# Performance work log

Hardware: AMD Instinct MI355X
Metric: run time of the kernel (lower is better)

Reference implementation:

```python
import jax, jax.numpy as jnp
import numpy as np

B, S, D, H = 1, 2048, 2048, 32
HD = D // H  # head_dim = 64
FF = 4 * D
EPS = 1e-5


def _alibi_slopes(n_heads):
    # standard ALiBi slopes for power-of-2 head counts: 2^(-8i/n)
    return np.array([2.0 ** (-8.0 * (i + 1) / n_heads) for i in range(n_heads)], np.float32)


def setup_inputs() -> dict:
    key = jax.random.key(0)
    ks = jax.random.split(key, 16)
    s = 0.02
    x = jax.random.normal(ks[0], (B, S, D), jnp.float32)
    # alibi bias [B, H, 1, S], broadcast over query positions (HF views alibi as (b, h, 1, kv_len))
    slopes = _alibi_slopes(H)
    alibi_np = slopes[:, None, None] * np.arange(S, dtype=np.float32)[None, None, :]
    alibi = jnp.broadcast_to(jnp.asarray(alibi_np), (B, H, 1, S))
    # additive causal mask [1, 1, S, S]
    causal = np.tril(np.ones((S, S), bool))
    attention_mask = jnp.asarray(np.where(causal, 0.0, -1e9).astype(np.float32))[None, None]
    p = lambda k, shp: s * jax.random.normal(k, shp, jnp.float32)
    return {
        "x": x,
        "alibi": alibi,
        "attention_mask": attention_mask,
        "ln1_g": jnp.ones((D,), jnp.float32), "ln1_b": jnp.zeros((D,), jnp.float32),
        "ln2_g": jnp.ones((D,), jnp.float32), "ln2_b": jnp.zeros((D,), jnp.float32),
        "wqkv": p(ks[1], (D, 3 * D)), "bqkv": jnp.zeros((3 * D,), jnp.float32),
        "wo": p(ks[2], (D, D)), "bo": jnp.zeros((D,), jnp.float32),
        "w1": p(ks[3], (D, FF)), "b1": jnp.zeros((FF,), jnp.float32),
        "w2": p(ks[4], (FF, D)), "b2": jnp.zeros((D,), jnp.float32),
    }


def _layernorm(h, g, b):
    m = h.mean(-1, keepdims=True)
    v = ((h - m) ** 2).mean(-1, keepdims=True)
    return (h - m) * jax.lax.rsqrt(v + EPS) * g + b


def reference(x, alibi, attention_mask, ln1_g, ln1_b, ln2_g, ln2_b,
              wqkv, bqkv, wo, bo, w1, b1, w2, b2):
    b, s, d = x.shape
    inv_norm = 1.0 / np.sqrt(HD).astype(np.float32)
    # --- input layernorm ---
    h = _layernorm(x, ln1_g, ln1_b)
    # --- fused QKV ---
    qkv = h @ wqkv + bqkv
    q, k, v = jnp.split(qkv, 3, axis=-1)
    q = q.reshape(b, s, H, HD).transpose(0, 2, 1, 3)  # [b, h, s, hd]
    k = k.reshape(b, s, H, HD).transpose(0, 2, 1, 3)
    v = v.reshape(b, s, H, HD).transpose(0, 2, 1, 3)
    # --- ALiBi-biased attention (HF falcon alibi path) ---
    scores = jnp.einsum("bhqd,bhkd->bhqk", q, k)          # [b, h, s, s]
    logits = (scores + alibi) * inv_norm + attention_mask  # alibi broadcasts over q dim
    probs = jax.nn.softmax(logits, axis=-1)
    ctx = jnp.einsum("bhqk,bhkd->bhqd", probs, v)
    ctx = ctx.transpose(0, 2, 1, 3).reshape(b, s, d)
    attn_out = ctx @ wo + bo
    # --- residual, post-attn layernorm, MLP (non-parallel falcon-rw layout) ---
    res = x + attn_out
    h2 = _layernorm(res, ln2_g, ln2_b)
    mlp = jax.nn.gelu(h2 @ w1 + b1, approximate=False) @ w2 + b2
    return res + mlp
```

## Files before the change

kernel.cpp:

```cpp
#include <hip/hip_runtime.h>
#include <hip/hip_bf16.h>
#include <cstdint>
#include <cstddef>

static constexpr int Sq  = 2048;
static constexpr int Dm  = 2048;
static constexpr int NH  = 32;
static constexpr int HDm = 64;
static constexpr int FFm = 8192;

typedef __bf16 bf16x8 __attribute__((ext_vector_type(8)));
typedef float  f32x4  __attribute__((ext_vector_type(4)));

__device__ __forceinline__ void async_ld16(const void* g, void* l) {
  __builtin_amdgcn_global_load_lds((const __attribute__((address_space(1))) void*)g,
                                   (__attribute__((address_space(3))) void*)l, 16, 0, 0);
}

__global__ __launch_bounds__(256)
void tcast_kernel(const float* __restrict__ in, __hip_bfloat16* __restrict__ out,
                  int K, int N) {
  __shared__ float tile[64][65];
  const int tc = blockIdx.x * 64;
  const int tr = blockIdx.y * 64;
  const int cx = threadIdx.x & 63;
  const int ry = threadIdx.x >> 6;
#pragma unroll
  for (int i = 0; i < 16; ++i) {
    int r = ry + i * 4;
    tile[r][cx] = in[(size_t)(tr + r) * N + tc + cx];
  }
  __syncthreads();
#pragma unroll
  for (int i = 0; i < 16; ++i) {
    int r = ry + i * 4;
    out[(size_t)(tc + r) * K + tr + cx] = __float2bfloat16(tile[cx][r]);
  }
}

__global__ __launch_bounds__(256)
void ln_kernel(const float* __restrict__ x, const float* __restrict__ g,
               const float* __restrict__ b, __hip_bfloat16* __restrict__ out) {
  __shared__ float red[4];
  const int t = threadIdx.x;
  const float* xr = x + (size_t)blockIdx.x * Dm;
  float v[8];
  float s = 0.f;
#pragma unroll
  for (int i = 0; i < 8; ++i) { v[i] = xr[t + i * 256]; s += v[i]; }
#pragma unroll
  for (int off = 32; off > 0; off >>= 1) s += __shfl_down(s, off, 64);
  if ((t & 63) == 0) red[t >> 6] = s;
  __syncthreads();
  const float mean = (red[0] + red[1] + red[2] + red[3]) * (1.f / Dm);
  __syncthreads();
  float vs = 0.f;
#pragma unroll
  for (int i = 0; i < 8; ++i) { float d = v[i] - mean; vs += d * d; }
#pragma unroll
  for (int off = 32; off > 0; off >>= 1) vs += __shfl_down(vs, off, 64);
  if ((t & 63) == 0) red[t >> 6] = vs;
  __syncthreads();
  const float inv = rsqrtf((red[0] + red[1] + red[2] + red[3]) * (1.f / Dm) + 1e-5f);
  __hip_bfloat16* orow = out + (size_t)blockIdx.x * Dm;
#pragma unroll
  for (int i = 0; i < 8; ++i) {
    int c = t + i * 256;
    orow[c] = __float2bfloat16((v[i] - mean) * inv * g[c] + b[c]);
  }
}

template <int EPI>
__global__ __launch_bounds__(256)
void gemm_kernel(const __hip_bfloat16* __restrict__ A,
                 const __hip_bfloat16* __restrict__ Bt,
                 int N, int K, int Ksub,
                 const float* __restrict__ bias,
                 const float* __restrict__ addsrc,
                 float* __restrict__ outf,
                 __hip_bfloat16* __restrict__ outb,
                 __hip_bfloat16* __restrict__ qo,
                 __hip_bfloat16* __restrict__ ko,
                 __hip_bfloat16* __restrict__ vo,
                 __hip_bfloat16* __restrict__ po) {
  __shared__ __align__(16) __hip_bfloat16 As[2][128 * 32];
  __shared__ __align__(16) __hip_bfloat16 Bs[2][128 * 32];
  const int t = threadIdx.x;
  const int lane = t & 63, w = t >> 6, quad = lane >> 4, l16 = lane & 15;
  const int bn = blockIdx.x, bm = blockIdx.y, bz = blockIdx.z;
  const int wm = (w & 1) * 64, wn = (w >> 1) * 64;
  const __hip_bfloat16* Abase = A + (size_t)bm * 128 * K;
  const __hip_bfloat16* Bbase = Bt + (size_t)bn * 128 * K;
  const int kBeg = bz * Ksub, kEnd = kBeg + Ksub;

  auto stage = [&](int b, int k0) {
#pragma unroll
    for (int j = 0; j < 2; ++j) {
      int c = j * 256 + t;
      int row = c >> 2;
      int p = c & 3;
      int g = (p - (row >> 1)) & 3;
      async_ld16(Abase + (size_t)row * K + k0 + g * 8, &As[b][c * 8]);
      async_ld16(Bbase + (size_t)row * K + k0 + g * 8, &Bs[b][c * 8]);
    }
  };

  f32x4 acc[4][4] = {};
  stage(0, kBeg);
  int buf = 0;
  for (int k0 = kBeg; k0 < kEnd; k0 += 32, buf ^= 1) {
    __syncthreads();
    if (k0 + 32 < kEnd) stage(buf ^ 1, k0 + 32);
    bf16x8 af[4], bfv[4];
#pragma unroll
    for (int i = 0; i < 4; ++i) {
      int row = wm + i * 16 + l16;
      int p = (quad + (row >> 1)) & 3;
      af[i] = *(const bf16x8*)(&As[buf][row * 32 + p * 8]);
    }
#pragma unroll
    for (int i = 0; i < 4; ++i) {
      int row = wn + i * 16 + l16;
      int p = (quad + (row >> 1)) & 3;
      bfv[i] = *(const bf16x8*)(&Bs[buf][row * 32 + p * 8]);
    }
#pragma unroll
    for (int mt = 0; mt < 4; ++mt)
#pragma unroll
      for (int nt = 0; nt < 4; ++nt)
        acc[mt][nt] = __builtin_amdgcn_mfma_f32_16x16x32_bf16(af[mt], bfv[nt], acc[mt][nt], 0, 0, 0);
  }
#pragma unroll
  for (int mt = 0; mt < 4; ++mt) {
#pragma unroll
    for (int nt = 0; nt < 4; ++nt) {
      const int n = bn * 128 + wn + nt * 16 + l16;
      const float bz2 = bias[n];
#pragma unroll
      for (int r = 0; r < 4; ++r) {
        const int m = bm * 128 + wm + mt * 16 + quad * 4 + r;
        float val = acc[mt][nt][r];
        if constexpr (EPI == 0) {
          val += bz2;
          int which = n >> 11, d2 = n & 2047;
          int hh = d2 >> 6, hd = d2 & 63;
          if (which == 0)
            qo[((size_t)hh * Sq + m) * HDm + hd] = __float2bfloat16(val * 0.125f);
          else if (which == 1)
            ko[((size_t)hh * Sq + m) * HDm + hd] = __float2bfloat16(val);
          else
            vo[((size_t)hh * HDm + hd) * Sq + m] = __float2bfloat16(val);
        } else if constexpr (EPI == 1) {
          outf[(size_t)m * N + n] = addsrc[(size_t)m * N + n] + bz2 + val;
        } else if constexpr (EPI == 2) {
          val += bz2;
          float gg = 0.5f * val * (1.0f + erff(val * 0.70710678118654752f));
          outb[(size_t)m * N + n] = __float2bfloat16(gg);
        } else {
          if (bz == 0)
            outf[(size_t)m * N + n] = addsrc[(size_t)m * N + n] + bz2 + val;
          else
            po[(size_t)m * N + n] = __float2bfloat16(val);
        }
      }
    }
  }
}

__global__ __launch_bounds__(256)
void addp_kernel(float* __restrict__ out, const __hip_bfloat16* __restrict__ p) {
  const int i = (blockIdx.x * 256 + threadIdx.x) * 4;
  float4 o = *(const float4*)(out + i);
  const __hip_bfloat16* pp = p + i;
  o.x += (float)pp[0]; o.y += (float)pp[1]; o.z += (float)pp[2]; o.w += (float)pp[3];
  *(float4*)(out + i) = o;
}

__global__ __launch_bounds__(256)
void attn_kernel(const __hip_bfloat16* __restrict__ qb,
                 const __hip_bfloat16* __restrict__ kb,
                 const __hip_bfloat16* __restrict__ vt,
                 const float* __restrict__ alibi,
                 __hip_bfloat16* __restrict__ ctx) {
  __shared__ __align__(16) __hip_bfloat16 Kl[2][64 * 64];
  __shared__ __align__(16) __hip_bfloat16 Vl[2][64 * 64];
  __shared__ __align__(16) __hip_bfloat16 Pl[4][16 * 64];
  const int pi = blockIdx.x, h = blockIdx.y;
  const int qA = pi, qB = (Sq / 64 - 1) - pi;
  const int t = threadIdx.x, w = t >> 6, lane = t & 63, quad = lane >> 4, l16 = lane & 15;
  const __hip_bfloat16* qh = qb + (size_t)h * Sq * HDm;
  const __hip_bfloat16* kh = kb + (size_t)h * Sq * HDm;
  const __hip_bfloat16* vh = vt + (size_t)h * HDm * Sq;
  const float* al = alibi + (size_t)h * Sq;

  const int rA = qA * 64 + w * 16 + l16;
  const int rB = qB * 64 + w * 16 + l16;
  const bf16x8 qA0 = *(const bf16x8*)(qh + (size_t)rA * HDm + quad * 8);
  const bf16x8 qA1 = *(const bf16x8*)(qh + (size_t)rA * HDm + 32 + quad * 8);
  const bf16x8 qB0 = *(const bf16x8*)(qh + (size_t)rB * HDm + quad * 8);
  const bf16x8 qB1 = *(const bf16x8*)(qh + (size_t)rB * HDm + 32 + quad * 8);

  auto stageS = [&](int b, int s) {
    const int kbk = (s <= qA) ? s : s - qA - 1;
#pragma unroll
    for (int j = 0; j < 2; ++j) {
      int c = j * 256 + t;
      int row = c >> 3;
      int swz = (c & 7) ^ (row & 7);
      async_ld16(kh + (size_t)(kbk * 64 + row) * HDm + swz * 8, &Kl[b][c * 8]);
      async_ld16(vh + (size_t)row * Sq + kbk * 64 + swz * 8, &Vl[b][c * 8]);
    }
  };

  f32x4 o[4] = {};
  float m_i[4], l_i[4];
#pragma unroll
  for (int r = 0; r < 4; ++r) { m_i[r] = -3e38f; l_i[r] = 0.f; }

  const int total = qA + qB + 2;
  stageS(0, 0);
  int buf = 0;
  for (int s = 0; s < total; ++s, buf ^= 1) {
    __syncthreads();
    if (s + 1 < total) stageS(buf ^ 1, s + 1);
    const bool ph = (s > qA);
    const int kbk = ph ? s - qA - 1 : s;
    const int qblk = ph ? qB : qA;
    const bf16x8 a0 = ph ? qB0 : qA0;
    const bf16x8 a1 = ph ? qB1 : qA1;

    f32x4 sf[4];
    const f32x4 zero = {};
#pragma unroll
    for (int nt = 0; nt < 4; ++nt) {
      int row = nt * 16 + l16;
      bf16x8 kf0 = *(const bf16x8*)(&Kl[buf][row * 64 + ((quad ^ (row & 7)) << 3)]);
      bf16x8 kf1 = *(const bf16x8*)(&Kl[buf][row * 64 + (((4 + quad) ^ (row & 7)) << 3)]);
      sf[nt] = __builtin_amdgcn_mfma_f32_16x16x32_bf16(a0, kf0, zero, 0, 0, 0);
      sf[nt] = __builtin_amdgcn_mfma_f32_16x16x32_bf16(a1, kf1, sf[nt], 0, 0, 0);
    }
    const bool diag = (kbk == qblk);
    float mrow[4] = {-3e38f, -3e38f, -3e38f, -3e38f};
#pragma unroll
    for (int nt = 0; nt < 4; ++nt) {
      const float ab = al[kbk * 64 + nt * 16 + l16] * 0.125f;
      const int kcol = nt * 16 + l16;
#pragma unroll
      for (int r = 0; r < 4; ++r) {
        float vv = sf[nt][r] + ab;
        if (diag && kcol > w * 16 + quad * 4 + r) vv = -3e38f;
        sf[nt][r] = vv;
        mrow[r] = fmaxf(mrow[r], vv);
      }
    }
#pragma unroll
    for (int off = 8; off > 0; off >>= 1)
#pragma unroll
      for (int r = 0; r < 4; ++r)
        mrow[r] = fmaxf(mrow[r], __shfl_xor(mrow[r], off, 64));
    float alpha[4], rs[4], p[4][4];
#pragma unroll
    for (int r = 0; r < 4; ++r) {
      float mn = fmaxf(m_i[r], mrow[r]);
      alpha[r] = __expf(m_i[r] - mn);
      m_i[r] = mn;
    }
#pragma unroll
    for (int nt = 0; nt < 4; ++nt)
#pragma unroll
      for (int r = 0; r < 4; ++r) p[nt][r] = __expf(sf[nt][r] - m_i[r]);
#pragma unroll
    for (int r = 0; r < 4; ++r) rs[r] = p[0][r] + p[1][r] + p[2][r] + p[3][r];
#pragma unroll
    for (int off = 8; off > 0; off >>= 1)
#pragma unroll
      for (int r = 0; r < 4; ++r) rs[r] += __shfl_xor(rs[r], off, 64);
#pragma unroll
    for (int r = 0; r < 4; ++r) l_i[r] = l_i[r] * alpha[r] + rs[r];
#pragma unroll
    for (int dt = 0; dt < 4; ++dt)
#pragma unroll
      for (int r = 0; r < 4; ++r) o[dt][r] *= alpha[r];
    __hip_bfloat16* pw = &Pl[w][0];
#pragma unroll
    for (int nt = 0; nt < 4; ++nt)
#pragma unroll
      for (int r = 0; r < 4; ++r) {
        int prow = quad * 4 + r;
        int e = nt * 16 + l16;
        int c16 = e >> 3;
        pw[prow * 64 + ((c16 ^ (prow & 7)) << 3) + (e & 7)] = __float2bfloat16(p[nt][r]);
      }
    asm volatile("s_waitcnt lgkmcnt(0)" ::: "memory");
    const bf16x8 pa0 = *(const bf16x8*)(pw + l16 * 64 + ((quad ^ (l16 & 7)) << 3));
    const bf16x8 pa1 = *(const bf16x8*)(pw + l16 * 64 + (((4 + quad) ^ (l16 & 7)) << 3));
#pragma unroll
    for (int dt = 0; dt < 4; ++dt) {
      int row = dt * 16 + l16;
      bf16x8 v0 = *(const bf16x8*)(&Vl[buf][row * 64 + ((quad ^ (row & 7)) << 3)]);
      bf16x8 v1 = *(const bf16x8*)(&Vl[buf][row * 64 + (((4 + quad) ^ (row & 7)) << 3)]);
      o[dt] = __builtin_amdgcn_mfma_f32_16x16x32_bf16(pa0, v0, o[dt], 0, 0, 0);
      o[dt] = __builtin_amdgcn_mfma_f32_16x16x32_bf16(pa1, v1, o[dt], 0, 0, 0);
    }
    if (s == qA) {
#pragma unroll
      for (int dt = 0; dt < 4; ++dt)
#pragma unroll
        for (int r = 0; r < 4; ++r) {
          int srow = qA * 64 + w * 16 + quad * 4 + r;
          ctx[(size_t)srow * Dm + h * HDm + dt * 16 + l16] =
              __float2bfloat16(o[dt][r] / l_i[r]);
          o[dt][r] = 0.f;
        }
#pragma unroll
      for (int r = 0; r < 4; ++r) { m_i[r] = -3e38f; l_i[r] = 0.f; }
    }
  }
#pragma unroll
  for (int dt = 0; dt < 4; ++dt)
#pragma unroll
    for (int r = 0; r < 4; ++r) {
      int srow = qB * 64 + w * 16 + quad * 4 + r;
      ctx[(size_t)srow * Dm + h * HDm + dt * 16 + l16] =
          __float2bfloat16(o[dt][r] / l_i[r]);
    }
}

extern "C" void kernel_launch(void* const* d_in, const int* in_sizes, int n_in,
                              void* d_out, int out_size, void* d_ws, size_t ws_size,
                              hipStream_t stream) {
  const float* x     = (const float*)d_in[0];
  const float* alibi = (const float*)d_in[1];
  const float* ln1g  = (const float*)d_in[3];
  const float* ln1b  = (const float*)d_in[4];
  const float* ln2g  = (const float*)d_in[5];
  const float* ln2b  = (const float*)d_in[6];
  const float* wqkv  = (const float*)d_in[7];
  const float* bqkv  = (const float*)d_in[8];
  const float* wo    = (const float*)d_in[9];
  const float* bo    = (const float*)d_in[10];
  const float* w1    = (const float*)d_in[11];
  const float* b1    = (const float*)d_in[12];
  const float* w2    = (const float*)d_in[13];
  const float* b2    = (const float*)d_in[14];
  float* out = (float*)d_out;

  char* p = (char*)d_ws;
  auto alloc = [&](size_t bytes) {
    char* r = p;
    p += (bytes + 255) & ~(size_t)255;
    return r;
  };
  constexpr size_t SD2 = (size_t)Sq * Dm * 2;
  char* R2 = alloc((size_t)FFm * Dm * 2);
  char* R1 = alloc(4 * SD2);
  __hip_bfloat16* hb   = (__hip_bfloat16*)alloc(SD2);
  float*          resb = (float*)alloc((size_t)Sq * Dm * 4);

  __hip_bfloat16* wqkvT = (__hip_bfloat16*)R2;
  __hip_bfloat16* w1T   = (__hip_bfloat16*)R2;
  __hip_bfloat16* w2T   = (__hip_bfloat16*)R2;
  __hip_bfloat16* qbuf  = (__hip_bfloat16*)(R1 + 0 * SD2);
  __hip_bfloat16* kbuf  = (__hip_bfloat16*)(R1 + 1 * SD2);
  __hip_bfloat16* vtbuf = (__hip_bfloat16*)(R1 + 2 * SD2);
  __hip_bfloat16* ctxb  = (__hip_bfloat16*)(R1 + 3 * SD2);
  __hip_bfloat16* woT   = (__hip_bfloat16*)(R1 + 0 * SD2);
  __hip_bfloat16* t1b   = (__hip_bfloat16*)R1;
  __hip_bfloat16* part  = hb;

  tcast_kernel<<<dim3(3 * Dm / 64, Dm / 64), 256, 0, stream>>>(wqkv, wqkvT, Dm, 3 * Dm);
  ln_kernel<<<Sq, 256, 0, stream>>>(x, ln1g, ln1b, hb);
  gemm_kernel<0><<<dim3(3 * Dm / 128, Sq / 128), 256, 0, stream>>>(
      hb, wqkvT, 3 * Dm, Dm, Dm, bqkv, nullptr, nullptr, nullptr, qbuf, kbuf, vtbuf, nullptr);
  tcast_kernel<<<dim3(FFm / 64, Dm / 64), 256, 0, stream>>>(w1, w1T, Dm, FFm);
  attn_kernel<<<dim3(Sq / 128, NH), 256, 0, stream>>>(qbuf, kbuf, vtbuf, alibi, ctxb);
  tcast_kernel<<<dim3(Dm / 64, Dm / 64), 256, 0, stream>>>(wo, woT, Dm, Dm);
  gemm_kernel<3><<<dim3(Dm / 128, Sq / 128, 2), 256, 0, stream>>>(
      ctxb, woT, Dm, Dm, Dm / 2, bo, x, resb, nullptr, nullptr, nullptr, nullptr, part);
  addp_kernel<<<(Sq * Dm) / 1024, 256, 0, stream>>>(resb, part);
  ln_kernel<<<Sq, 256, 0, stream>>>(resb, ln2g, ln2b, hb);
  gemm_kernel<2><<<dim3(FFm / 128, Sq / 128), 256, 0, stream>>>(
      hb, w1T, FFm, Dm, Dm, b1, nullptr, nullptr, t1b, nullptr, nullptr, nullptr, nullptr);
  tcast_kernel<<<dim3(Dm / 64, FFm / 64), 256, 0, stream>>>(w2, w2T, FFm, Dm);
  gemm_kernel<3><<<dim3(Dm / 128, Sq / 128, 2), 256, 0, stream>>>(
      t1b, w2T, Dm, FFm, FFm / 2, b2, resb, out, nullptr, nullptr, nullptr, nullptr, part);
  addp_kernel<<<(Sq * Dm) / 1024, 256, 0, stream>>>(out, part);
}
```

Before: 674.6 us.

## Register-staged GEMM prefetch pipeline with XCD-aware block remapping

Replaces the direct global-to-LDS async loads with loads into registers that are written to shared memory one step later. The K loop is unrolled by two, and each barrier waits only on LDS counters, so global loads stay in flight across the MFMA compute. Block indices are also remapped so that groups of adjacent tiles land on the same XCD, aiming for better L2 reuse. In exchange this costs more registers. The remap hardcodes 16 M-blocks and assumes the grid divides evenly by 8.

```diff
diff --git a/kernel.cpp b/kernel.cpp
--- a/kernel.cpp
+++ b/kernel.cpp
@@ -87,49 +87,81 @@
   __shared__ __align__(16) __hip_bfloat16 Bs[2][128 * 32];
   const int t = threadIdx.x;
   const int lane = t & 63, w = t >> 6, quad = lane >> 4, l16 = lane & 15;
-  const int bn = blockIdx.x, bm = blockIdx.y, bz = blockIdx.z;
+  const int nbx = gridDim.x;
+  const int id = blockIdx.y * nbx + blockIdx.x;
+  const int chunk = (nbx * 16) >> 3;
+  const int nid = (id & 7) * chunk + (id >> 3);
+  const int bn = nid >> 4, bm = nid & 15;
+  const int bz = blockIdx.z;
   const int wm = (w & 1) * 64, wn = (w >> 1) * 64;
   const __hip_bfloat16* Abase = A + (size_t)bm * 128 * K;
   const __hip_bfloat16* Bbase = Bt + (size_t)bn * 128 * K;
-  const int kBeg = bz * Ksub, kEnd = kBeg + Ksub;
-
-  auto stage = [&](int b, int k0) {
-#pragma unroll
-    for (int j = 0; j < 2; ++j) {
-      int c = j * 256 + t;
-      int row = c >> 2;
-      int p = c & 3;
-      int g = (p - (row >> 1)) & 3;
-      async_ld16(Abase + (size_t)row * K + k0 + g * 8, &As[b][c * 8]);
-      async_ld16(Bbase + (size_t)row * K + k0 + g * 8, &Bs[b][c * 8]);
-    }
+  const int kBeg = bz * Ksub;
+  const int kSteps = Ksub / 32;
+
+  const int c0 = t, c1 = t + 256;
+  const int r0 = c0 >> 2, g0 = ((c0 & 3) - (r0 >> 1)) & 3;
+  const int r1 = c1 >> 2, g1 = ((c1 & 3) - (r1 >> 1)) & 3;
+  const __hip_bfloat16* a0p = Abase + (size_t)r0 * K + g0 * 8;
+  const __hip_bfloat16* a1p = Abase + (size_t)r1 * K + g1 * 8;
+  const __hip_bfloat16* b0p = Bbase + (size_t)r0 * K + g0 * 8;
+  const __hip_bfloat16* b1p = Bbase + (size_t)r1 * K + g1 * 8;
+
+  struct Stage { bf16x8 a0, a1, b0, b1; };
+  auto gload = [&](int k0) {
+    Stage s;
+    s.a0 = *(const bf16x8*)(a0p + k0);
+    s.a1 = *(const bf16x8*)(a1p + k0);
+    s.b0 = *(const bf16x8*)(b0p + k0);
+    s.b1 = *(const bf16x8*)(b1p + k0);
+    return s;
   };
+  auto swrite = [&](int b, const Stage& s) {
+    *(bf16x8*)(&As[b][c0 * 8]) = s.a0;
+    *(bf16x8*)(&As[b][c1 * 8]) = s.a1;
+    *(bf16x8*)(&Bs[b][c0 * 8]) = s.b0;
+    *(bf16x8*)(&Bs[b][c1 * 8]) = s.b1;
+  };
 
   f32x4 acc[4][4] = {};
-  stage(0, kBeg);
-  int buf = 0;
-  for (int k0 = kBeg; k0 < kEnd; k0 += 32, buf ^= 1) {
-    __syncthreads();
-    if (k0 + 32 < kEnd) stage(buf ^ 1, k0 + 32);
+  auto compute = [&](int b) {
     bf16x8 af[4], bfv[4];
 #pragma unroll
     for (int i = 0; i < 4; ++i) {
       int row = wm + i * 16 + l16;
       int p = (quad + (row >> 1)) & 3;
-      af[i] = *(const bf16x8*)(&As[buf][row * 32 + p * 8]);
+      af[i] = *(const bf16x8*)(&As[b][row * 32 + p * 8]);
     }
 #pragma unroll
     for (int i = 0; i < 4; ++i) {
       int row = wn + i * 16 + l16;
       int p = (quad + (row >> 1)) & 3;
-      bfv[i] = *(const bf16x8*)(&Bs[buf][row * 32 + p * 8]);
+      bfv[i] = *(const bf16x8*)(&Bs[b][row * 32 + p * 8]);
     }
 #pragma unroll
     for (int mt = 0; mt < 4; ++mt)
 #pragma unroll
       for (int nt = 0; nt < 4; ++nt)
         acc[mt][nt] = __builtin_amdgcn_mfma_f32_16x16x32_bf16(af[mt], bfv[nt], acc[mt][nt], 0, 0, 0);
-  }
+  };
+
+#define BAR() asm volatile("s_waitcnt lgkmcnt(0)\ns_barrier" ::: "memory")
+  Stage s0 = gload(kBeg);
+  Stage s1 = gload(kBeg + 32);
+  swrite(0, s0);
+  BAR();
+  for (int i = 0; i < kSteps; i += 2) {
+    if (i + 2 < kSteps) s0 = gload(kBeg + (i + 2) * 32);
+    compute(0);
+    swrite(1, s1);
+    BAR();
+    if (i + 3 < kSteps) s1 = gload(kBeg + (i + 3) * 32);
+    compute(1);
+    if (i + 2 < kSteps) swrite(0, s0);
+    BAR();
+  }
+#undef BAR
+
 #pragma unroll
   for (int mt = 0; mt < 4; ++mt) {
 #pragma unroll
```

Measured after the change: 652.6 us. 1.03x faster.

## Single-buffer GEMM, add 64-row tile variant, and swizzle block order

Applied to the files above, without the earlier changes.

The GEMM kernel gains a tile-height template parameter. The Wo, W1 and W2 GEMMs now use 64x128 tiles with more blocks and a higher occupancy hint. LDS double buffering is replaced by a single buffer that is loaded and synchronized twice per k-step, and the linear block id is remapped so consecutive blocks spread across groups of 8, which is meant to improve L2 locality. This trades prefetch overlap for occupancy. The smaller tiles also reduce A/B reuse per block.

```diff
diff --git a/kernel.cpp b/kernel.cpp
--- a/kernel.cpp
+++ b/kernel.cpp
@@ -70,8 +70,8 @@
   }
 }
 
-template <int EPI>
-__global__ __launch_bounds__(256)
+template <int EPI, int MT>
+__global__ __launch_bounds__(256, MT == 64 ? 4 : 3)
 void gemm_kernel(const __hip_bfloat16* __restrict__ A,
                  const __hip_bfloat16* __restrict__ Bt,
                  int N, int K, int Ksub,
@@ -83,62 +83,68 @@
                  __hip_bfloat16* __restrict__ ko,
                  __hip_bfloat16* __restrict__ vo,
                  __hip_bfloat16* __restrict__ po) {
-  __shared__ __align__(16) __hip_bfloat16 As[2][128 * 32];
-  __shared__ __align__(16) __hip_bfloat16 Bs[2][128 * 32];
+  __shared__ __align__(16) __hip_bfloat16 As[MT * 32];
+  __shared__ __align__(16) __hip_bfloat16 Bs[128 * 32];
   const int t = threadIdx.x;
   const int lane = t & 63, w = t >> 6, quad = lane >> 4, l16 = lane & 15;
-  const int bn = blockIdx.x, bm = blockIdx.y, bz = blockIdx.z;
-  const int wm = (w & 1) * 64, wn = (w >> 1) * 64;
-  const __hip_bfloat16* Abase = A + (size_t)bm * 128 * K;
+  const int nbx = gridDim.x, nby = gridDim.y;
+  const int id = blockIdx.y * nbx + blockIdx.x;
+  const int total = nbx * nby;
+  const int nid = (id & 7) * (total >> 3) + (id >> 3);
+  const int lb = __ffs(nby) - 1;
+  const int bm = nid & (nby - 1), bn = nid >> lb;
+  const int bz = blockIdx.z;
+  const int wm = (MT == 128) ? (w & 1) * 64 : 0;
+  const int wn = (MT == 128) ? (w >> 1) * 64 : w * 32;
+  constexpr int NTI = (MT == 128) ? 4 : 2;
+  const __hip_bfloat16* Abase = A + (size_t)bm * MT * K;
   const __hip_bfloat16* Bbase = Bt + (size_t)bn * 128 * K;
   const int kBeg = bz * Ksub, kEnd = kBeg + Ksub;
 
-  auto stage = [&](int b, int k0) {
-#pragma unroll
-    for (int j = 0; j < 2; ++j) {
-      int c = j * 256 + t;
-      int row = c >> 2;
-      int p = c & 3;
-      int g = (p - (row >> 1)) & 3;
-      async_ld16(Abase + (size_t)row * K + k0 + g * 8, &As[b][c * 8]);
-      async_ld16(Bbase + (size_t)row * K + k0 + g * 8, &Bs[b][c * 8]);
-    }
-  };
-
-  f32x4 acc[4][4] = {};
-  stage(0, kBeg);
-  int buf = 0;
-  for (int k0 = kBeg; k0 < kEnd; k0 += 32, buf ^= 1) {
+  const int row0 = t >> 2;
+  const int g0 = ((t & 3) - (row0 >> 1)) & 3;
+  const __hip_bfloat16* aptr0 = Abase + (size_t)row0 * K + g0 * 8 + kBeg;
+  const __hip_bfloat16* aptr1 = Abase + (size_t)(row0 + 64) * K + g0 * 8 + kBeg;
+  const __hip_bfloat16* bptr0 = Bbase + (size_t)row0 * K + g0 * 8 + kBeg;
+  const __hip_bfloat16* bptr1 = Bbase + (size_t)(row0 + 64) * K + g0 * 8 + kBeg;
+
+  f32x4 acc[4][NTI] = {};
+  for (int k0 = 0; k0 < kEnd - kBeg; k0 += 32) {
     __syncthreads();
-    if (k0 + 32 < kEnd) stage(buf ^ 1, k0 + 32);
-    bf16x8 af[4], bfv[4];
+    async_ld16(aptr0 + k0, &As[t * 8]);
+    if constexpr (MT == 128) async_ld16(aptr1 + k0, &As[(t + 256) * 8]);
+    async_ld16(bptr0 + k0, &Bs[t * 8]);
+    async_ld16(bptr1 + k0, &Bs[(t + 256) * 8]);
+    __syncthreads();
+    bf16x8 af[4], bfv[NTI];
 #pragma unroll
     for (int i = 0; i < 4; ++i) {
       int row = wm + i * 16 + l16;
       int p = (quad + (row >> 1)) & 3;
-      af[i] = *(const bf16x8*)(&As[buf][row * 32 + p * 8]);
-    }
-#pragma unroll
-    for (int i = 0; i < 4; ++i) {
+      af[i] = *(const bf16x8*)(&As[row * 32 + p * 8]);
+    }
+#pragma unroll
+    for (int i = 0; i < NTI; ++i) {
       int row = wn + i * 16 + l16;
       int p = (quad + (row >> 1)) & 3;
-      bfv[i] = *(const bf16x8*)(&Bs[buf][row * 32 + p * 8]);
+      bfv[i] = *(const bf16x8*)(&Bs[row * 32 + p * 8]);
     }
 #pragma unroll
     for (int mt = 0; mt < 4; ++mt)
 #pragma unroll
-      for (int nt = 0; nt < 4; ++nt)
+      for (int nt = 0; nt < NTI; ++nt)
         acc[mt][nt] = __builtin_amdgcn_mfma_f32_16x16x32_bf16(af[mt], bfv[nt], acc[mt][nt], 0, 0, 0);
   }
+
 #pragma unroll
   for (int mt = 0; mt < 4; ++mt) {
 #pragma unroll
-    for (int nt = 0; nt < 4; ++nt) {
+    for (int nt = 0; nt < NTI; ++nt) {
       const int n = bn * 128 + wn + nt * 16 + l16;
       const float bz2 = bias[n];
 #pragma unroll
       for (int r = 0; r < 4; ++r) {
-        const int m = bm * 128 + wm + mt * 16 + quad * 4 + r;
+        const int m = bm * MT + wm + mt * 16 + quad * 4 + r;
         float val = acc[mt][nt][r];
         if constexpr (EPI == 0) {
           val += bz2;
@@ -150,8 +156,6 @@
             ko[((size_t)hh * Sq + m) * HDm + hd] = __float2bfloat16(val);
           else
             vo[((size_t)hh * HDm + hd) * Sq + m] = __float2bfloat16(val);
-        } else if constexpr (EPI == 1) {
-          outf[(size_t)m * N + n] = addsrc[(size_t)m * N + n] + bz2 + val;
         } else if constexpr (EPI == 2) {
           val += bz2;
           float gg = 0.5f * val * (1.0f + erff(val * 0.70710678118654752f));
@@ -370,19 +374,19 @@
 
   tcast_kernel<<<dim3(3 * Dm / 64, Dm / 64), 256, 0, stream>>>(wqkv, wqkvT, Dm, 3 * Dm);
   ln_kernel<<<Sq, 256, 0, stream>>>(x, ln1g, ln1b, hb);
-  gemm_kernel<0><<<dim3(3 * Dm / 128, Sq / 128), 256, 0, stream>>>(
+  gemm_kernel<0, 128><<<dim3(3 * Dm / 128, Sq / 128), 256, 0, stream>>>(
       hb, wqkvT, 3 * Dm, Dm, Dm, bqkv, nullptr, nullptr, nullptr, qbuf, kbuf, vtbuf, nullptr);
   tcast_kernel<<<dim3(FFm / 64, Dm / 64), 256, 0, stream>>>(w1, w1T, Dm, FFm);
   attn_kernel<<<dim3(Sq / 128, NH), 256, 0, stream>>>(qbuf, kbuf, vtbuf, alibi, ctxb);
   tcast_kernel<<<dim3(Dm / 64, Dm / 64), 256, 0, stream>>>(wo, woT, Dm, Dm);
-  gemm_kernel<3><<<dim3(Dm / 128, Sq / 128, 2), 256, 0, stream>>>(
+  gemm_kernel<3, 64><<<dim3(Dm / 128, Sq / 64, 2), 256, 0, stream>>>(
       ctxb, woT, Dm, Dm, Dm / 2, bo, x, resb, nullptr, nullptr, nullptr, nullptr, part);
   addp_kernel<<<(Sq * Dm) / 1024, 256, 0, stream>>>(resb, part);
   ln_kernel<<<Sq, 256, 0, stream>>>(resb, ln2g, ln2b, hb);
-  gemm_kernel<2><<<dim3(FFm / 128, Sq / 128), 256, 0, stream>>>(
+  gemm_kernel<2, 64><<<dim3(FFm / 128, Sq / 64), 256, 0, stream>>>(
       hb, w1T, FFm, Dm, Dm, b1, nullptr, nullptr, t1b, nullptr, nullptr, nullptr, nullptr);
   tcast_kernel<<<dim3(Dm / 64, FFm / 64), 256, 0, stream>>>(w2, w2T, FFm, Dm);
-  gemm_kernel<3><<<dim3(Dm / 128, Sq / 128, 2), 256, 0, stream>>>(
+  gemm_kernel<3, 64><<<dim3(Dm / 128, Sq / 64, 2), 256, 0, stream>>>(
       t1b, w2T, Dm, FFm, FFm / 2, b2, resb, out, nullptr, nullptr, nullptr, nullptr, part);
   addp_kernel<<<(Sq * Dm) / 1024, 256, 0, stream>>>(out, part);
 }
```

Result: slower. 697.4 us (+3.4%).
